# Performance work log

Hardware: AMD Instinct MI355X
Metric: run time of the kernel (lower is better)

The kernel has to match this reference:

```python
import jax, jax.numpy as jnp
import numpy as np

D = 512          # input_dim == hidden size of MinLSTM layers
OUT = 1          # output_dim of fc_out
B, T = 8, 4096
LN_EPS = 1e-5


def _linear_params(key, d_in, d_out):
    kw, kb = jax.random.split(key)
    lim = 1.0 / np.sqrt(d_in)
    W = jax.random.uniform(kw, (d_out, d_in), minval=-lim, maxval=lim, dtype=jnp.float32)
    b = jax.random.uniform(kb, (d_out,), minval=-lim, maxval=lim, dtype=jnp.float32)
    return W, b


def setup_inputs() -> dict:
    key = jax.random.key(0)
    ks = jax.random.split(key, 8)
    x = jax.random.normal(ks[0], (B, T, D), dtype=jnp.float32)
    Wf0, bf0 = _linear_params(ks[1], D, D)
    Wi0, bi0 = _linear_params(ks[2], D, D)
    Wh0, bh0 = _linear_params(ks[3], D, D)
    Wf1, bf1 = _linear_params(ks[4], D, D)
    Wi1, bi1 = _linear_params(ks[5], D, D)
    Wh1, bh1 = _linear_params(ks[6], D, D)
    W_out, b_out = _linear_params(ks[7], D, OUT)
    ln_g = jnp.ones((D,), dtype=jnp.float32)
    ln_b = jnp.zeros((D,), dtype=jnp.float32)
    return {
        'x': x,
        'Wf0': Wf0, 'bf0': bf0, 'Wi0': Wi0, 'bi0': bi0, 'Wh0': Wh0, 'bh0': bh0,
        'Wf1': Wf1, 'bf1': bf1, 'Wi1': Wi1, 'bi1': bi1, 'Wh1': Wh1, 'bh1': bh1,
        'ln_g': ln_g, 'ln_b': ln_b, 'W_out': W_out, 'b_out': b_out,
    }


def _minlstm(x, Wf, bf, Wi, bi, Wh, bh):
    # minLSTM (parallel form, h0 = 0):
    #   f = sigma(W_f x), i = sigma(W_i x), h~ = W_h x
    #   f' = f/(f+i), i' = i/(f+i)
    #   h_t = f'_t * h_{t-1} + i'_t * h~_t   (linear recurrence -> associative scan)
    f = jax.nn.sigmoid(jnp.einsum('btd,ed->bte', x, Wf) + bf)
    i = jax.nn.sigmoid(jnp.einsum('btd,ed->bte', x, Wi) + bi)
    h_tilde = jnp.einsum('btd,ed->bte', x, Wh) + bh
    denom = f + i
    a = f / denom                      # decay coefficient f'
    u = (i / denom) * h_tilde          # input contribution i' * h~

    def combine(c1, c2):
        a1, u1 = c1
        a2, u2 = c2
        return a1 * a2, a2 * u1 + u2

    _, h = jax.lax.associative_scan(combine, (a, u), axis=1)
    return h  # [B, T, D]


def reference(x, Wf0, bf0, Wi0, bi0, Wh0, bh0,
              Wf1, bf1, Wi1, bi1, Wh1, bh1,
              ln_g, ln_b, W_out, b_out):
    h = _minlstm(x, Wf0, bf0, Wi0, bi0, Wh0, bh0)
    h = _minlstm(h, Wf1, bf1, Wi1, bi1, Wh1, bh1)
    h = jnp.where(jnp.isnan(h), x, h)      # NaN fallback to input
    h = x + h                               # residual
    # LayerNorm over last dim
    mu = jnp.mean(h, axis=-1, keepdims=True)
    var = jnp.mean(jnp.square(h - mu), axis=-1, keepdims=True)
    hn = (h - mu) * jax.lax.rsqrt(var + LN_EPS) * ln_g + ln_b
    # output projection [B, T, OUT]
    return jnp.einsum('btd,od->bto', hn, W_out) + b_out
```

## Files before the change

### kernel.cpp

```cpp
#include <hip/hip_runtime.h>
#include <hip/hip_bf16.h>
#include <stdint.h>


#define MROWS 32768
#define DDIM  512
#define TLEN  4096
#define BSZ   8
#define NCHUNK 64
#define CLEN   64

typedef __attribute__((ext_vector_type(8))) __bf16 bf16x8;
typedef __attribute__((ext_vector_type(4))) float f32x4;
typedef __attribute__((ext_vector_type(4))) unsigned short ushort4_t;
typedef __attribute__((ext_vector_type(2))) unsigned short ushort2_t;

static __device__ __forceinline__ unsigned short f2bf(float f) {
    unsigned int u = __float_as_uint(f);
    u = (u + 0x7FFFu + ((u >> 16) & 1u)) >> 16;
    return (unsigned short)u;
}
static __device__ __forceinline__ float bf2f(unsigned short s) {
    return __uint_as_float(((unsigned int)s) << 16);
}
static __device__ __forceinline__ void gload_lds16(const void* gptr, void* ldsp) {
    __builtin_amdgcn_global_load_lds(
        (const __attribute__((address_space(1))) uint32_t*)gptr,
        (__attribute__((address_space(3))) uint32_t*)ldsp,
        16, 0, 0);
}

__global__ __launch_bounds__(256) void cast_all(
    const float4* __restrict__ x,
    const float4* __restrict__ w0, const float4* __restrict__ w1,
    const float4* __restrict__ w2, const float4* __restrict__ w3,
    const float4* __restrict__ w4, const float4* __restrict__ w5,
    ushort4_t* __restrict__ xb, ushort4_t* __restrict__ wb)
{
    int i = blockIdx.x * 256 + threadIdx.x;
    float4 v;
    ushort4_t* dst;
    if (i < 4194304) {
        v = x[i];
        dst = xb + i;
    } else {
        int j = i - 4194304;
        int wsel = j >> 16;
        int rem = j & 65535;
        const float4* src = (wsel == 0) ? w0 : (wsel == 1) ? w1 : (wsel == 2) ? w2
                          : (wsel == 3) ? w3 : (wsel == 4) ? w4 : w5;
        v = src[rem];
        dst = wb + j;
    }
    ushort4_t o;
    o.x = f2bf(v.x); o.y = f2bf(v.y); o.z = f2bf(v.z); o.w = f2bf(v.w);
    *dst = o;
}

__global__ __launch_bounds__(256) void gates_gemm(
    const unsigned short* __restrict__ X,
    const unsigned short* __restrict__ Wf,
    const unsigned short* __restrict__ Wi,
    const unsigned short* __restrict__ Wh,
    const float* __restrict__ bf_, const float* __restrict__ bi_,
    const float* __restrict__ bh_,
    unsigned short* __restrict__ a_out, unsigned short* __restrict__ u_out)
{
    __shared__ __align__(16) unsigned short lds[2 * 20480];

    const int tid  = threadIdx.x;
    const int lane = tid & 63;
    const int wave = tid >> 6;
    const int wm = wave >> 1, wn = wave & 1;
    const int lr  = lane & 15;
    const int kgl = lane >> 4;

    const int w = blockIdx.x;
    const int xcd = w & 7;
    const int s = w >> 3;
    const int by = xcd * 32 + (s >> 3);
    const int bx = s & 7;
    const int mblk = by * 128;
    const int nblk = bx * 64;

    const int srow = tid >> 3;
    const int scol = ((tid & 7) ^ (srow & 7)) << 3;
    const unsigned short* pA = X  + (size_t)(mblk + srow) * 512 + scol;
    const unsigned short* pF = Wf + (size_t)(nblk + srow) * 512 + scol;
    const unsigned short* pI = Wi + (size_t)(nblk + srow) * 512 + scol;
    const unsigned short* pH = Wh + (size_t)(nblk + srow) * 512 + scol;

    int aoff[4], boff[2];
#pragma unroll
    for (int mi = 0; mi < 4; ++mi) {
        int row = wm * 64 + mi * 16 + lr;
        aoff[mi] = row * 64 + ((kgl ^ (row & 7)) << 3);
    }
#pragma unroll
    for (int ni = 0; ni < 2; ++ni) {
        int row = wn * 32 + ni * 16 + lr;
        boff[ni] = row * 64 + ((kgl ^ (row & 7)) << 3);
    }

    f32x4 accF[4][2], accI[4][2], accH[4][2];
    const f32x4 zero = {0.f, 0.f, 0.f, 0.f};
#pragma unroll
    for (int mi = 0; mi < 4; ++mi)
#pragma unroll
        for (int ni = 0; ni < 2; ++ni) {
            accF[mi][ni] = zero; accI[mi][ni] = zero; accH[mi][ni] = zero;
        }

#define STAGE(buf) do { \
    gload_lds16(pA,            (buf) + wave * 512);             \
    gload_lds16(pA + 32 * 512, (buf) + 2048  + wave * 512);     \
    gload_lds16(pA + 64 * 512, (buf) + 4096  + wave * 512);     \
    gload_lds16(pA + 96 * 512, (buf) + 6144  + wave * 512);     \
    gload_lds16(pF,            (buf) + 8192  + wave * 512);     \
    gload_lds16(pF + 32 * 512, (buf) + 10240 + wave * 512);     \
    gload_lds16(pI,            (buf) + 12288 + wave * 512);     \
    gload_lds16(pI + 32 * 512, (buf) + 14336 + wave * 512);     \
    gload_lds16(pH,            (buf) + 16384 + wave * 512);     \
    gload_lds16(pH + 32 * 512, (buf) + 18432 + wave * 512);     \
    pA += 64; pF += 64; pI += 64; pH += 64; } while (0)

    STAGE(lds);

    for (int t = 0; t < 8; ++t) {
        unsigned short* cbuf = lds + (t & 1) * 20480;
        unsigned short* nbuf = lds + ((t & 1) ^ 1) * 20480;
        if (t < 7) {
            STAGE(nbuf);
            asm volatile("s_waitcnt vmcnt(10)" ::: "memory");
        } else {
            asm volatile("s_waitcnt vmcnt(0)" ::: "memory");
        }
        __builtin_amdgcn_s_barrier();
        __builtin_amdgcn_sched_barrier(0);

#pragma unroll
        for (int ks = 0; ks < 2; ++ks) {
            const int kx = ks << 5;
            bf16x8 af[4];
#pragma unroll
            for (int mi = 0; mi < 4; ++mi)
                af[mi] = *reinterpret_cast<const bf16x8*>(cbuf + (aoff[mi] ^ kx));
            bf16x8 bF[2], bI[2], bH[2];
#pragma unroll
            for (int ni = 0; ni < 2; ++ni) {
                bF[ni] = *reinterpret_cast<const bf16x8*>(cbuf + 8192  + (boff[ni] ^ kx));
                bI[ni] = *reinterpret_cast<const bf16x8*>(cbuf + 12288 + (boff[ni] ^ kx));
                bH[ni] = *reinterpret_cast<const bf16x8*>(cbuf + 16384 + (boff[ni] ^ kx));
            }
            __builtin_amdgcn_s_setprio(1);
#pragma unroll
            for (int mi = 0; mi < 4; ++mi)
#pragma unroll
                for (int ni = 0; ni < 2; ++ni) {
                    accF[mi][ni] = __builtin_amdgcn_mfma_f32_16x16x32_bf16(af[mi], bF[ni], accF[mi][ni], 0, 0, 0);
                    accI[mi][ni] = __builtin_amdgcn_mfma_f32_16x16x32_bf16(af[mi], bI[ni], accI[mi][ni], 0, 0, 0);
                    accH[mi][ni] = __builtin_amdgcn_mfma_f32_16x16x32_bf16(af[mi], bH[ni], accH[mi][ni], 0, 0, 0);
                }
            __builtin_amdgcn_s_setprio(0);
        }
        __builtin_amdgcn_sched_barrier(0);
        __builtin_amdgcn_s_barrier();
        __builtin_amdgcn_sched_barrier(0);
    }
#undef STAGE

#pragma unroll
    for (int ni = 0; ni < 2; ++ni) {
        const int n = nblk + wn * 32 + ni * 16 + lr;
        const float bfv = bf_[n], biv = bi_[n], bhv = bh_[n];
#pragma unroll
        for (int mi = 0; mi < 4; ++mi) {
#pragma unroll
            for (int r = 0; r < 4; ++r) {
                const int m = mblk + wm * 64 + mi * 16 + kgl * 4 + r;
                float zf = accF[mi][ni][r] + bfv;
                float zi = accI[mi][ni][r] + biv;
                float zh = accH[mi][ni][r] + bhv;
                float fv = 1.0f / (1.0f + __expf(-zf));
                float iv = 1.0f / (1.0f + __expf(-zi));
                float dn = fv + iv;
                size_t idx = (size_t)m * 512 + n;
                a_out[idx] = f2bf(fv / dn);
                u_out[idx] = f2bf((iv / dn) * zh);
            }
        }
    }
}

__global__ void scan_pass1(const ushort4_t* __restrict__ a, const ushort4_t* __restrict__ u,
                           float4* __restrict__ Asum, float4* __restrict__ Usum) {
    int gid = blockIdx.x * 256 + threadIdx.x;
    int d4 = gid & 127;
    int c  = (gid >> 7) & 63;
    int b  = gid >> 13;
    size_t base = (size_t)(b * TLEN + c * CLEN) * 128 + d4;
    float A[4] = {1.f, 1.f, 1.f, 1.f};
    float h[4] = {0.f, 0.f, 0.f, 0.f};
#pragma unroll 4
    for (int l = 0; l < CLEN; ++l) {
        ushort4_t av4 = a[base + (size_t)l * 128];
        ushort4_t uv4 = u[base + (size_t)l * 128];
#pragma unroll
        for (int j = 0; j < 4; ++j) {
            float av = bf2f(av4[j]), uv = bf2f(uv4[j]);
            A[j] *= av;
            h[j] = av * h[j] + uv;
        }
    }
    size_t s4 = (size_t)(b * NCHUNK + c) * 128 + d4;
    Asum[s4] = make_float4(A[0], A[1], A[2], A[3]);
    Usum[s4] = make_float4(h[0], h[1], h[2], h[3]);
}

__global__ void scan_pass2(const float4* __restrict__ Asum, const float4* __restrict__ Usum,
                           float4* __restrict__ Hinit) {
    int t = blockIdx.x * 256 + threadIdx.x;
    int d4 = t & 127;
    int b = t >> 7;
    float4 h = {0.f, 0.f, 0.f, 0.f};
    for (int c = 0; c < NCHUNK; ++c) {
        size_t idx = (size_t)(b * NCHUNK + c) * 128 + d4;
        Hinit[idx] = h;
        float4 A = Asum[idx]; float4 U = Usum[idx];
        h.x = A.x * h.x + U.x; h.y = A.y * h.y + U.y;
        h.z = A.z * h.z + U.z; h.w = A.w * h.w + U.w;
    }
}

__global__ void scan_pass3(const ushort4_t* __restrict__ a, const ushort4_t* __restrict__ u,
                           const float4* __restrict__ Hinit,
                           ushort4_t* __restrict__ hout) {
    int gid = blockIdx.x * 256 + threadIdx.x;
    int d4 = gid & 127;
    int c  = (gid >> 7) & 63;
    int b  = gid >> 13;
    size_t base = (size_t)(b * TLEN + c * CLEN) * 128 + d4;
    size_t s4 = (size_t)(b * NCHUNK + c) * 128 + d4;
    float4 h0 = Hinit[s4];
    float h[4] = {h0.x, h0.y, h0.z, h0.w};
#pragma unroll 4
    for (int l = 0; l < CLEN; ++l) {
        size_t idx = base + (size_t)l * 128;
        ushort4_t av4 = a[idx];
        ushort4_t uv4 = u[idx];
        ushort4_t o;
#pragma unroll
        for (int j = 0; j < 4; ++j) {
            float av = bf2f(av4[j]), uv = bf2f(uv4[j]);
            h[j] = av * h[j] + uv;
            o[j] = f2bf(h[j]);
        }
        hout[idx] = o;
    }
}

__global__ __launch_bounds__(256) void final_kernel(
    const float* __restrict__ x, const unsigned short* __restrict__ h1,
    const float* __restrict__ g, const float* __restrict__ bvec,
    const float* __restrict__ Wout, const float* __restrict__ bout,
    float* __restrict__ out)
{
    int row = blockIdx.x;
    int tid = threadIdx.x;
    size_t base = (size_t)row * 512;
    ushort2_t hv2 = *reinterpret_cast<const ushort2_t*>(h1 + base + tid * 2);
    float2 xv2 = *reinterpret_cast<const float2*>(x + base + tid * 2);
    float r[2];
#pragma unroll
    for (int j = 0; j < 2; ++j) {
        float hv = bf2f(hv2[j]);
        float xv = (j == 0) ? xv2.x : xv2.y;
        if (hv != hv) hv = xv;
        r[j] = xv + hv;
    }
    float s = r[0] + r[1];
    float q = r[0] * r[0] + r[1] * r[1];
#pragma unroll
    for (int m = 32; m >= 1; m >>= 1) {
        s += __shfl_xor(s, m);
        q += __shfl_xor(q, m);
    }
    __shared__ float ss[4], sq[4], sp[4];
    int w = tid >> 6, lane = tid & 63;
    if (lane == 0) { ss[w] = s; sq[w] = q; }
    __syncthreads();
    float tot  = ss[0] + ss[1] + ss[2] + ss[3];
    float totq = sq[0] + sq[1] + sq[2] + sq[3];
    float mu = tot * (1.0f / 512.0f);
    float var = totq * (1.0f / 512.0f) - mu * mu;
    float rstd = rsqrtf(var + 1e-5f);
    float p = 0.0f;
#pragma unroll
    for (int j = 0; j < 2; ++j) {
        int d = tid * 2 + j;
        float nv = (r[j] - mu) * rstd * g[d] + bvec[d];
        p += nv * Wout[d];
    }
#pragma unroll
    for (int m = 32; m >= 1; m >>= 1) p += __shfl_xor(p, m);
    if (lane == 0) sp[w] = p;
    __syncthreads();
    if (tid == 0) out[row] = sp[0] + sp[1] + sp[2] + sp[3] + bout[0];
}

extern "C" void kernel_launch(void* const* d_in, const int* in_sizes, int n_in,
                              void* d_out, int out_size, void* d_ws, size_t ws_size,
                              hipStream_t stream) {
    const float* x    = (const float*)d_in[0];
    const float* Wf0  = (const float*)d_in[1];  const float* bf0 = (const float*)d_in[2];
    const float* Wi0  = (const float*)d_in[3];  const float* bi0 = (const float*)d_in[4];
    const float* Wh0  = (const float*)d_in[5];  const float* bh0 = (const float*)d_in[6];
    const float* Wf1  = (const float*)d_in[7];  const float* bf1 = (const float*)d_in[8];
    const float* Wi1  = (const float*)d_in[9];  const float* bi1 = (const float*)d_in[10];
    const float* Wh1  = (const float*)d_in[11]; const float* bh1 = (const float*)d_in[12];
    const float* ln_g = (const float*)d_in[13]; const float* ln_b = (const float*)d_in[14];
    const float* W_out = (const float*)d_in[15]; const float* b_out = (const float*)d_in[16];

    char* ws = (char*)d_ws;
    unsigned short* Xb = (unsigned short*)ws;  ws += (size_t)MROWS * DDIM * 2;
    unsigned short* Wball = (unsigned short*)ws;
    unsigned short* Wb[6];
    for (int i = 0; i < 6; ++i) { Wb[i] = (unsigned short*)ws; ws += (size_t)DDIM * DDIM * 2; }
    unsigned short* abuf = (unsigned short*)ws; ws += (size_t)MROWS * DDIM * 2;
    unsigned short* ubuf = (unsigned short*)ws; ws += (size_t)MROWS * DDIM * 2;
    float* Asum = (float*)ws;  ws += (size_t)BSZ * NCHUNK * DDIM * 4;
    float* Usum = (float*)ws;  ws += (size_t)BSZ * NCHUNK * DDIM * 4;
    float* Hinit = (float*)ws; ws += (size_t)BSZ * NCHUNK * DDIM * 4;
    unsigned short* h0b = (unsigned short*)ws; ws += (size_t)MROWS * DDIM * 2;
    unsigned short* h1b = (unsigned short*)ws; ws += (size_t)MROWS * DDIM * 2;

    cast_all<<<17920, 256, 0, stream>>>(
        (const float4*)x, (const float4*)Wf0, (const float4*)Wi0, (const float4*)Wh0,
        (const float4*)Wf1, (const float4*)Wi1, (const float4*)Wh1,
        (ushort4_t*)Xb, (ushort4_t*)Wball);

    gates_gemm<<<2048, 256, 0, stream>>>(Xb, Wb[0], Wb[1], Wb[2], bf0, bi0, bh0, abuf, ubuf);
    scan_pass1<<<256, 256, 0, stream>>>((const ushort4_t*)abuf, (const ushort4_t*)ubuf,
                                        (float4*)Asum, (float4*)Usum);
    scan_pass2<<<4, 256, 0, stream>>>((const float4*)Asum, (const float4*)Usum, (float4*)Hinit);
    scan_pass3<<<256, 256, 0, stream>>>((const ushort4_t*)abuf, (const ushort4_t*)ubuf,
                                        (const float4*)Hinit, (ushort4_t*)h0b);

    gates_gemm<<<2048, 256, 0, stream>>>(h0b, Wb[3], Wb[4], Wb[5], bf1, bi1, bh1, abuf, ubuf);
    scan_pass1<<<256, 256, 0, stream>>>((const ushort4_t*)abuf, (const ushort4_t*)ubuf,
                                        (float4*)Asum, (float4*)Usum);
    scan_pass2<<<4, 256, 0, stream>>>((const float4*)Asum, (const float4*)Usum, (float4*)Hinit);
    scan_pass3<<<256, 256, 0, stream>>>((const ushort4_t*)abuf, (const ushort4_t*)ubuf,
                                        (const float4*)Hinit, (ushort4_t*)h1b);

    final_kernel<<<MROWS, 256, 0, stream>>>(x, h1b, ln_g, ln_b, W_out, b_out, (float*)d_out);
}
```

Baseline: 250.1 us.

## Widen gates GEMM tile, deepen LDS pipeline, and interleave a/u output

The gates GEMM moves to 512-thread blocks computing 128x128 output tiles, with a 4-buffer LDS ring over K-steps of 32, three stages kept in flight and a single barrier per step. The a and u gate outputs are packed into one 32-bit word per element, so the scan passes issue one 16-byte load instead of two 8-byte loads. The aim is fewer loads of X per output, better overlap of loads with MFMA work, and wider memory accesses in the scans. The cost is higher register and LDS use per block, and the single barrier per step relies on the ring depth to avoid overwriting a buffer that is still being read.

After: 281.4 us. 12.5% more time.

```diff
diff --git a/kernel.cpp b/kernel.cpp
--- a/kernel.cpp
+++ b/kernel.cpp
@@ -29,6 +29,8 @@
         (__attribute__((address_space(3))) uint32_t*)ldsp,
         16, 0, 0);
 }
+
+#define WAITV(n) asm volatile("s_waitcnt vmcnt(" #n ")" ::: "memory")
 
 __global__ __launch_bounds__(256) void cast_all(
     const float4* __restrict__ x,
@@ -57,49 +59,50 @@
     *dst = o;
 }
 
-__global__ __launch_bounds__(256) void gates_gemm(
+__global__ __launch_bounds__(512, 2) void gates_gemm(
     const unsigned short* __restrict__ X,
     const unsigned short* __restrict__ Wf,
     const unsigned short* __restrict__ Wi,
     const unsigned short* __restrict__ Wh,
     const float* __restrict__ bf_, const float* __restrict__ bi_,
     const float* __restrict__ bh_,
-    unsigned short* __restrict__ a_out, unsigned short* __restrict__ u_out)
+    unsigned int* __restrict__ au_out)
 {
-    __shared__ __align__(16) unsigned short lds[2 * 20480];
+    __shared__ __align__(16) unsigned short lds[4 * 16384];
 
     const int tid  = threadIdx.x;
     const int lane = tid & 63;
     const int wave = tid >> 6;
-    const int wm = wave >> 1, wn = wave & 1;
+    const int wm = wave >> 2, wn = wave & 3;
     const int lr  = lane & 15;
     const int kgl = lane >> 4;
 
     const int w = blockIdx.x;
     const int xcd = w & 7;
     const int s = w >> 3;
-    const int by = xcd * 32 + (s >> 3);
-    const int bx = s & 7;
+    const int by = xcd * 32 + (s >> 2);
+    const int bx = s & 3;
     const int mblk = by * 128;
-    const int nblk = bx * 64;
-
-    const int srow = tid >> 3;
-    const int scol = ((tid & 7) ^ (srow & 7)) << 3;
-    const unsigned short* pA = X  + (size_t)(mblk + srow) * 512 + scol;
-    const unsigned short* pF = Wf + (size_t)(nblk + srow) * 512 + scol;
-    const unsigned short* pI = Wi + (size_t)(nblk + srow) * 512 + scol;
-    const unsigned short* pH = Wh + (size_t)(nblk + srow) * 512 + scol;
+    const int nblk = bx * 128;
+
+    const int srow = tid >> 2;
+    const int sg   = ((tid & 3) ^ (srow & 3)) << 3;
+    const int tid8 = tid * 8;
+    const unsigned short* pA = X  + (size_t)(mblk + srow) * 512 + sg;
+    const unsigned short* pF = Wf + (size_t)(nblk + srow) * 512 + sg;
+    const unsigned short* pI = Wi + (size_t)(nblk + srow) * 512 + sg;
+    const unsigned short* pH = Wh + (size_t)(nblk + srow) * 512 + sg;
 
     int aoff[4], boff[2];
 #pragma unroll
     for (int mi = 0; mi < 4; ++mi) {
         int row = wm * 64 + mi * 16 + lr;
-        aoff[mi] = row * 64 + ((kgl ^ (row & 7)) << 3);
+        aoff[mi] = row * 32 + (((kgl ^ row) & 3) << 3) + ((kgl & ~3) << 3);
     }
 #pragma unroll
     for (int ni = 0; ni < 2; ++ni) {
         int row = wn * 32 + ni * 16 + lr;
-        boff[ni] = row * 64 + ((kgl ^ (row & 7)) << 3);
+        boff[ni] = row * 32 + (((kgl ^ row) & 3) << 3) + ((kgl & ~3) << 3);
     }
 
     f32x4 accF[4][2], accI[4][2], accH[4][2];
@@ -111,61 +114,49 @@
             accF[mi][ni] = zero; accI[mi][ni] = zero; accH[mi][ni] = zero;
         }
 
-#define STAGE(buf) do { \
-    gload_lds16(pA,            (buf) + wave * 512);             \
-    gload_lds16(pA + 32 * 512, (buf) + 2048  + wave * 512);     \
-    gload_lds16(pA + 64 * 512, (buf) + 4096  + wave * 512);     \
-    gload_lds16(pA + 96 * 512, (buf) + 6144  + wave * 512);     \
-    gload_lds16(pF,            (buf) + 8192  + wave * 512);     \
-    gload_lds16(pF + 32 * 512, (buf) + 10240 + wave * 512);     \
-    gload_lds16(pI,            (buf) + 12288 + wave * 512);     \
-    gload_lds16(pI + 32 * 512, (buf) + 14336 + wave * 512);     \
-    gload_lds16(pH,            (buf) + 16384 + wave * 512);     \
-    gload_lds16(pH + 32 * 512, (buf) + 18432 + wave * 512);     \
-    pA += 64; pF += 64; pI += 64; pH += 64; } while (0)
+#define STAGE(bufp) do { \
+    gload_lds16(pA, (bufp) + tid8);          \
+    gload_lds16(pF, (bufp) + 4096 + tid8);   \
+    gload_lds16(pI, (bufp) + 8192 + tid8);   \
+    gload_lds16(pH, (bufp) + 12288 + tid8);  \
+    pA += 32; pF += 32; pI += 32; pH += 32; } while (0)
 
     STAGE(lds);
-
-    for (int t = 0; t < 8; ++t) {
-        unsigned short* cbuf = lds + (t & 1) * 20480;
-        unsigned short* nbuf = lds + ((t & 1) ^ 1) * 20480;
-        if (t < 7) {
-            STAGE(nbuf);
-            asm volatile("s_waitcnt vmcnt(10)" ::: "memory");
-        } else {
-            asm volatile("s_waitcnt vmcnt(0)" ::: "memory");
-        }
+    STAGE(lds + 16384);
+    STAGE(lds + 32768);
+
+#pragma unroll
+    for (int t = 0; t < 16; ++t) {
+        if (t <= 13) { WAITV(8); }
+        else if (t == 14) { WAITV(4); }
+        else { WAITV(0); }
         __builtin_amdgcn_s_barrier();
         __builtin_amdgcn_sched_barrier(0);
 
-#pragma unroll
-        for (int ks = 0; ks < 2; ++ks) {
-            const int kx = ks << 5;
-            bf16x8 af[4];
-#pragma unroll
-            for (int mi = 0; mi < 4; ++mi)
-                af[mi] = *reinterpret_cast<const bf16x8*>(cbuf + (aoff[mi] ^ kx));
-            bf16x8 bF[2], bI[2], bH[2];
+        if (t < 13) STAGE(lds + ((t + 3) & 3) * 16384);
+
+        const unsigned short* cb = lds + (t & 3) * 16384;
+        bf16x8 af[4];
+#pragma unroll
+        for (int mi = 0; mi < 4; ++mi)
+            af[mi] = *reinterpret_cast<const bf16x8*>(cb + aoff[mi]);
+        bf16x8 bF[2], bI[2], bH[2];
+#pragma unroll
+        for (int ni = 0; ni < 2; ++ni) {
+            bF[ni] = *reinterpret_cast<const bf16x8*>(cb + 4096  + boff[ni]);
+            bI[ni] = *reinterpret_cast<const bf16x8*>(cb + 8192  + boff[ni]);
+            bH[ni] = *reinterpret_cast<const bf16x8*>(cb + 12288 + boff[ni]);
+        }
+        __builtin_amdgcn_s_setprio(1);
+#pragma unroll
+        for (int mi = 0; mi < 4; ++mi)
 #pragma unroll
             for (int ni = 0; ni < 2; ++ni) {
-                bF[ni] = *reinterpret_cast<const bf16x8*>(cbuf + 8192  + (boff[ni] ^ kx));
-                bI[ni] = *reinterpret_cast<const bf16x8*>(cbuf + 12288 + (boff[ni] ^ kx));
-                bH[ni] = *reinterpret_cast<const bf16x8*>(cbuf + 16384 + (boff[ni] ^ kx));
+                accF[mi][ni] = __builtin_amdgcn_mfma_f32_16x16x32_bf16(af[mi], bF[ni], accF[mi][ni], 0, 0, 0);
+                accI[mi][ni] = __builtin_amdgcn_mfma_f32_16x16x32_bf16(af[mi], bI[ni], accI[mi][ni], 0, 0, 0);
+                accH[mi][ni] = __builtin_amdgcn_mfma_f32_16x16x32_bf16(af[mi], bH[ni], accH[mi][ni], 0, 0, 0);
             }
-            __builtin_amdgcn_s_setprio(1);
-#pragma unroll
-            for (int mi = 0; mi < 4; ++mi)
-#pragma unroll
-                for (int ni = 0; ni < 2; ++ni) {
-                    accF[mi][ni] = __builtin_amdgcn_mfma_f32_16x16x32_bf16(af[mi], bF[ni], accF[mi][ni], 0, 0, 0);
-                    accI[mi][ni] = __builtin_amdgcn_mfma_f32_16x16x32_bf16(af[mi], bI[ni], accI[mi][ni], 0, 0, 0);
-                    accH[mi][ni] = __builtin_amdgcn_mfma_f32_16x16x32_bf16(af[mi], bH[ni], accH[mi][ni], 0, 0, 0);
-                }
-            __builtin_amdgcn_s_setprio(0);
-        }
-        __builtin_amdgcn_sched_barrier(0);
-        __builtin_amdgcn_s_barrier();
-        __builtin_amdgcn_sched_barrier(0);
+        __builtin_amdgcn_s_setprio(0);
     }
 #undef STAGE
 
@@ -184,15 +175,16 @@
                 float fv = 1.0f / (1.0f + __expf(-zf));
                 float iv = 1.0f / (1.0f + __expf(-zi));
                 float dn = fv + iv;
-                size_t idx = (size_t)m * 512 + n;
-                a_out[idx] = f2bf(fv / dn);
-                u_out[idx] = f2bf((iv / dn) * zh);
+                float av = fv / dn;
+                float uv = (iv / dn) * zh;
+                au_out[(size_t)m * 512 + n] =
+                    ((unsigned int)f2bf(uv) << 16) | (unsigned int)f2bf(av);
             }
         }
     }
 }
 
-__global__ void scan_pass1(const ushort4_t* __restrict__ a, const ushort4_t* __restrict__ u,
+__global__ void scan_pass1(const uint4* __restrict__ au,
                            float4* __restrict__ Asum, float4* __restrict__ Usum) {
     int gid = blockIdx.x * 256 + threadIdx.x;
     int d4 = gid & 127;
@@ -203,11 +195,12 @@
     float h[4] = {0.f, 0.f, 0.f, 0.f};
 #pragma unroll 4
     for (int l = 0; l < CLEN; ++l) {
-        ushort4_t av4 = a[base + (size_t)l * 128];
-        ushort4_t uv4 = u[base + (size_t)l * 128];
+        uint4 v = au[base + (size_t)l * 128];
+        unsigned int vv[4] = {v.x, v.y, v.z, v.w};
 #pragma unroll
         for (int j = 0; j < 4; ++j) {
-            float av = bf2f(av4[j]), uv = bf2f(uv4[j]);
+            float av = __uint_as_float(vv[j] << 16);
+            float uv = __uint_as_float(vv[j] & 0xFFFF0000u);
             A[j] *= av;
             h[j] = av * h[j] + uv;
         }
@@ -232,7 +225,7 @@
     }
 }
 
-__global__ void scan_pass3(const ushort4_t* __restrict__ a, const ushort4_t* __restrict__ u,
+__global__ void scan_pass3(const uint4* __restrict__ au,
                            const float4* __restrict__ Hinit,
                            ushort4_t* __restrict__ hout) {
     int gid = blockIdx.x * 256 + threadIdx.x;
@@ -246,12 +239,13 @@
 #pragma unroll 4
     for (int l = 0; l < CLEN; ++l) {
         size_t idx = base + (size_t)l * 128;
-        ushort4_t av4 = a[idx];
-        ushort4_t uv4 = u[idx];
+        uint4 v = au[idx];
+        unsigned int vv[4] = {v.x, v.y, v.z, v.w};
         ushort4_t o;
 #pragma unroll
         for (int j = 0; j < 4; ++j) {
-            float av = bf2f(av4[j]), uv = bf2f(uv4[j]);
+            float av = __uint_as_float(vv[j] << 16);
+            float uv = __uint_as_float(vv[j] & 0xFFFF0000u);
             h[j] = av * h[j] + uv;
             o[j] = f2bf(h[j]);
         }
@@ -326,8 +320,7 @@
     unsigned short* Wball = (unsigned short*)ws;
     unsigned short* Wb[6];
     for (int i = 0; i < 6; ++i) { Wb[i] = (unsigned short*)ws; ws += (size_t)DDIM * DDIM * 2; }
-    unsigned short* abuf = (unsigned short*)ws; ws += (size_t)MROWS * DDIM * 2;
-    unsigned short* ubuf = (unsigned short*)ws; ws += (size_t)MROWS * DDIM * 2;
+    unsigned int* aubuf = (unsigned int*)ws; ws += (size_t)MROWS * DDIM * 4;
     float* Asum = (float*)ws;  ws += (size_t)BSZ * NCHUNK * DDIM * 4;
     float* Usum = (float*)ws;  ws += (size_t)BSZ * NCHUNK * DDIM * 4;
     float* Hinit = (float*)ws; ws += (size_t)BSZ * NCHUNK * DDIM * 4;
@@ -339,19 +332,15 @@
         (const float4*)Wf1, (const float4*)Wi1, (const float4*)Wh1,
         (ushort4_t*)Xb, (ushort4_t*)Wball);
 
-    gates_gemm<<<2048, 256, 0, stream>>>(Xb, Wb[0], Wb[1], Wb[2], bf0, bi0, bh0, abuf, ubuf);
-    scan_pass1<<<256, 256, 0, stream>>>((const ushort4_t*)abuf, (const ushort4_t*)ubuf,
-                                        (float4*)Asum, (float4*)Usum);
+    gates_gemm<<<1024, 512, 0, stream>>>(Xb, Wb[0], Wb[1], Wb[2], bf0, bi0, bh0, aubuf);
+    scan_pass1<<<256, 256, 0, stream>>>((const uint4*)aubuf, (float4*)Asum, (float4*)Usum);
     scan_pass2<<<4, 256, 0, stream>>>((const float4*)Asum, (const float4*)Usum, (float4*)Hinit);
-    scan_pass3<<<256, 256, 0, stream>>>((const ushort4_t*)abuf, (const ushort4_t*)ubuf,
-                                        (const float4*)Hinit, (ushort4_t*)h0b);
-
-    gates_gemm<<<2048, 256, 0, stream>>>(h0b, Wb[3], Wb[4], Wb[5], bf1, bi1, bh1, abuf, ubuf);
-    scan_pass1<<<256, 256, 0, stream>>>((const ushort4_t*)abuf, (const ushort4_t*)ubuf,
-                                        (float4*)Asum, (float4*)Usum);
+    scan_pass3<<<256, 256, 0, stream>>>((const uint4*)aubuf, (const float4*)Hinit, (ushort4_t*)h0b);
+
+    gates_gemm<<<1024, 512, 0, stream>>>(h0b, Wb[3], Wb[4], Wb[5], bf1, bi1, bh1, aubuf);
+    scan_pass1<<<256, 256, 0, stream>>>((const uint4*)aubuf, (float4*)Asum, (float4*)Usum);
     scan_pass2<<<4, 256, 0, stream>>>((const float4*)Asum, (const float4*)Usum, (float4*)Hinit);
-    scan_pass3<<<256, 256, 0, stream>>>((const ushort4_t*)abuf, (const ushort4_t*)ubuf,
-                                        (const float4*)Hinit, (ushort4_t*)h1b);
+    scan_pass3<<<256, 256, 0, stream>>>((const uint4*)aubuf, (const float4*)Hinit, (ushort4_t*)h1b);
 
     final_kernel<<<MROWS, 256, 0, stream>>>(x, h1b, ln_g, ln_b, W_out, b_out, (float*)d_out);
 }
```
